# Optimization experiments

Measured on AMD Instinct MI355X. Metric: run time of the kernel, lower is better.

## Reference

```python
import jax, jax.numpy as jnp
import numpy as np

B, N, DIN = 1, 1024, 512
NF, DCOND, H = 4, 128, 8
HD = DIN // H


def layernorm(x, g, b, eps=1e-5):
    mu = jnp.mean(x, axis=-1, keepdims=True)
    var = jnp.var(x, axis=-1, keepdims=True)
    return (x - mu) * jax.lax.rsqrt(var + eps) * g + b


def modlin2d(x, code, w_c, ln_g, ln_b, W, b):
    # code: [dcond, nf]; w_c: [din, dcond] -> code_mod: [nf, 1, din]
    code_mod = layernorm((w_c @ code).T, ln_g, ln_b)[:, None, :]
    return jnp.matmul(x * code_mod, W.T) + b


def setup_inputs() -> dict:
    key = jax.random.key(0)
    ks = jax.random.split(key, 8)
    s = lambda d: 1.0 / np.sqrt(d)
    return {
        "x": jax.random.normal(ks[0], (B, N, DIN), jnp.float32),
        "compatibility": jax.random.uniform(ks[1], (B, NF, N), jnp.float32),
        "code": jax.random.normal(ks[2], (DCOND, NF), jnp.float32),
        "w_c": jax.random.normal(ks[3], (DIN, DCOND), jnp.float32) * s(DCOND),
        "W_qkv": jax.random.normal(ks[4], (3 * DIN, DIN), jnp.float32) * s(DIN),
        "b_qkv": jnp.zeros((3 * DIN,), jnp.float32),
        "W_proj": jax.random.normal(ks[5], (DIN, DIN), jnp.float32) * s(DIN),
        "b_proj": jnp.zeros((DIN,), jnp.float32),
        "ln_qkv_g": jnp.ones((DIN,), jnp.float32),
        "ln_qkv_b": jnp.zeros((DIN,), jnp.float32),
        "ln_proj_g": jnp.ones((DIN,), jnp.float32),
        "ln_proj_b": jnp.zeros((DIN,), jnp.float32),
    }


def reference(x, compatibility, code, w_c, W_qkv, b_qkv, W_proj, b_proj,
              ln_qkv_g, ln_qkv_b, ln_proj_g, ln_proj_b):
    b, n, e = x.shape
    hd = e // H
    scale = hd ** -0.5
    # QKV: [B, nf, N, 3*din] -> split into [3, B, H, nf, N, hd]
    qkv = modlin2d(x[:, None, :, :], code, w_c, ln_qkv_g, ln_qkv_b, W_qkv, b_qkv)
    qkv = qkv.reshape(b, NF, n, 3, H, hd).transpose(3, 0, 4, 1, 2, 5)
    q, k, v = qkv[0], qkv[1], qkv[2]
    # first softmax over scaled scores
    attn = jax.nn.softmax(jnp.einsum('bhfnd,bhfmd->bhfnm', q, k) * scale, axis=-1)
    # compatibility outer product: [B, N, N] (sums over function axis)
    compat = jnp.einsum('bfn,bfm->bnm', compatibility, compatibility)
    W_hat = attn * compat[:, None, None, :, :]
    # second softmax
    Wm = jax.nn.softmax(W_hat, axis=-1)
    y_hat = jnp.einsum('bhfnm,bhfmd->bhfnd', Wm, v)
    y_hat = y_hat.transpose(0, 2, 3, 1, 4).reshape(b, NF, n, e)
    y = modlin2d(y_hat, code, w_c, ln_proj_g, ln_proj_b, W_proj, b_proj)
    return y
```

## Files before the change

### kernel.cpp

```cpp
#include <hip/hip_runtime.h>
#include <hip/hip_bf16.h>
#include <math.h>

#define NTOK 1024
#define DIN  512
#define NF   4
#define DCOND 128
#define H    8
#define HD   64
#define NQKV 1536
#define LOG2E 1.4426950408889634f

typedef __attribute__((ext_vector_type(8))) short bf16x8;
typedef __attribute__((ext_vector_type(4))) float f32x4;
typedef __attribute__((ext_vector_type(4))) unsigned short us4;

__device__ __forceinline__ unsigned short f2b(float f) {
  union { float f; unsigned int u; } v; v.f = f;
  unsigned int r = v.u + 0x7fffu + ((v.u >> 16) & 1u);
  return (unsigned short)(r >> 16);
}

__device__ __forceinline__ float b2f(unsigned short h) {
  union { unsigned int u; float f; } v; v.u = ((unsigned int)h) << 16;
  return v.f;
}

__device__ __forceinline__ float asf(unsigned int u) {
  union { unsigned int u; float f; } v; v.u = u;
  return v.f;
}

__device__ __forceinline__ void gl_lds16(const void* g, void* l) {
  __builtin_amdgcn_global_load_lds(
      (const __attribute__((address_space(1))) unsigned int*)g,
      (__attribute__((address_space(3))) unsigned int*)l, 16, 0, 0);
}

__global__ void ln_kernel(const float* __restrict__ code, const float* __restrict__ w_c,
                          const float* __restrict__ lnqg, const float* __restrict__ lnqb,
                          const float* __restrict__ lnpg, const float* __restrict__ lnpb,
                          float* __restrict__ cmq, float* __restrict__ cmp_) {
  const int i = threadIdx.x;
  const int w = i >> 6, lane = i & 63;
  float t[NF] = {0.f, 0.f, 0.f, 0.f};
  const float* wr = w_c + i * DCOND;
#pragma unroll 8
  for (int k = 0; k < DCOND; k += 4) {
    float4 wv = *reinterpret_cast<const float4*>(wr + k);
    float4 c0 = *reinterpret_cast<const float4*>(&code[k * 4]);
    float4 c1 = *reinterpret_cast<const float4*>(&code[(k + 1) * 4]);
    float4 c2 = *reinterpret_cast<const float4*>(&code[(k + 2) * 4]);
    float4 c3 = *reinterpret_cast<const float4*>(&code[(k + 3) * 4]);
    t[0] += wv.x * c0.x + wv.y * c1.x + wv.z * c2.x + wv.w * c3.x;
    t[1] += wv.x * c0.y + wv.y * c1.y + wv.z * c2.y + wv.w * c3.y;
    t[2] += wv.x * c0.z + wv.y * c1.z + wv.z * c2.z + wv.w * c3.z;
    t[3] += wv.x * c0.w + wv.y * c1.w + wv.z * c2.w + wv.w * c3.w;
  }
  __shared__ float redS[8], redQ[8];
#pragma unroll
  for (int f = 0; f < NF; ++f) {
    float s = t[f], q = t[f] * t[f];
#pragma unroll
    for (int o = 32; o > 0; o >>= 1) { s += __shfl_xor(s, o); q += __shfl_xor(q, o); }
    if (lane == 0) { redS[w] = s; redQ[w] = q; }
    __syncthreads();
    float S = 0.f, Q = 0.f;
#pragma unroll
    for (int j = 0; j < 8; ++j) { S += redS[j]; Q += redQ[j]; }
    float mu = S * (1.f / 512.f);
    float var = Q * (1.f / 512.f) - mu * mu;
    float rstd = rsqrtf(var + 1e-5f);
    float nv = (t[f] - mu) * rstd;
    cmq[f * DIN + i]  = nv * lnqg[i] + lnqb[i];
    cmp_[f * DIN + i] = nv * lnpg[i] + lnpb[i];
    __syncthreads();
  }
}

__global__ void prep2_kernel(const float* __restrict__ W_qkv, const float* __restrict__ W_proj,
                             const float* __restrict__ x, const float* __restrict__ cmq,
                             unsigned short* __restrict__ Wqh, unsigned short* __restrict__ Wph,
                             unsigned short* __restrict__ xm) {
  const int bid = blockIdx.x, tid = threadIdx.x;
  if (bid < 256) {
    const float* src; unsigned short* dst; int e;
    if (bid < 192) { src = W_qkv; dst = Wqh; e = bid * 4096 + tid * 16; }
    else { src = W_proj; dst = Wph; e = (bid - 192) * 4096 + tid * 16; }
#pragma unroll
    for (int j = 0; j < 4; ++j) {
      float4 a = *reinterpret_cast<const float4*>(&src[e + j * 4]);
      us4 p = { f2b(a.x), f2b(a.y), f2b(a.z), f2b(a.w) };
      *reinterpret_cast<us4*>(&dst[e + j * 4]) = p;
    }
  } else {
    int e = (bid - 256) * 4096 + tid * 16;
    int row = e >> 9, d = e & 511;
    int f = row >> 10, n = row & 1023;
    const float* xr = x + (size_t)n * DIN + d;
    const float* cr = cmq + f * DIN + d;
#pragma unroll
    for (int j = 0; j < 4; ++j) {
      float4 a = *reinterpret_cast<const float4*>(xr + j * 4);
      float4 c = *reinterpret_cast<const float4*>(cr + j * 4);
      us4 p = { f2b(a.x * c.x), f2b(a.y * c.y), f2b(a.z * c.z), f2b(a.w * c.w) };
      *reinterpret_cast<us4*>(&xm[e + j * 4]) = p;
    }
  }
}

template<int NCOL, bool OUT_BF16, bool WRITE_VT, bool SCALE_Q>
__global__ __launch_bounds__(256, 6)
void gemm64(const unsigned short* __restrict__ Ah,
            const unsigned short* __restrict__ Wh,
            const float* __restrict__ bias,
            unsigned short* __restrict__ outH,
            float* __restrict__ outF,
            unsigned short* __restrict__ vT) {
  __shared__ __align__(16) unsigned short sA[2][2048];
  __shared__ __align__(16) unsigned short sB[2][2048];
  const int tid = threadIdx.x;
  const int lane = tid & 63, w = tid >> 6;
  const int li = lane & 15, g = lane >> 4;
  const int wr = (w >> 1) * 32, wc = (w & 1) * 32;
  const int row0 = blockIdx.y * 64, col0 = blockIdx.x * 64;
  const int f = row0 >> 10;
  const int sr = tid >> 2, sp = tid & 3;
  const int ss = sp ^ ((sr >> 1) & 3);

  f32x4 acc[2][2];
#pragma unroll
  for (int m = 0; m < 2; ++m)
#pragma unroll
    for (int n = 0; n < 2; ++n) acc[m][n] = (f32x4){0.f, 0.f, 0.f, 0.f};

  const unsigned short* aSrc = Ah + (size_t)(row0 + sr) * DIN + ss * 8;
  const unsigned short* bSrc = Wh + (size_t)(col0 + sr) * DIN + ss * 8;

  gl_lds16(aSrc, &sA[0][w * 512]);
  gl_lds16(bSrc, &sB[0][w * 512]);
  __syncthreads();
  for (int it = 0; it < 16; ++it) {
    int buf = it & 1;
    if (it < 15) {
      gl_lds16(aSrc + (it + 1) * 32, &sA[buf ^ 1][w * 512]);
      gl_lds16(bSrc + (it + 1) * 32, &sB[buf ^ 1][w * 512]);
    }
    bf16x8 aF[2], bF[2];
#pragma unroll
    for (int m = 0; m < 2; ++m) {
      int ra = wr + m * 16 + li;
      aF[m] = *reinterpret_cast<const bf16x8*>(&sA[buf][(ra * 4 + (g ^ ((ra >> 1) & 3))) * 8]);
    }
#pragma unroll
    for (int n = 0; n < 2; ++n) {
      int cb = wc + n * 16 + li;
      bF[n] = *reinterpret_cast<const bf16x8*>(&sB[buf][(cb * 4 + (g ^ ((cb >> 1) & 3))) * 8]);
    }
#pragma unroll
    for (int m = 0; m < 2; ++m)
#pragma unroll
      for (int n = 0; n < 2; ++n)
        acc[m][n] = __builtin_amdgcn_mfma_f32_16x16x32_bf16(aF[m], bF[n], acc[m][n], 0, 0, 0);
    __syncthreads();
  }
#pragma unroll
  for (int n = 0; n < 2; ++n) {
    int col = col0 + wc + n * 16 + li;
    float bb = bias[col];
    float sc = (SCALE_Q && col < DIN) ? (0.125f * LOG2E) : 1.0f;
#pragma unroll
    for (int m = 0; m < 2; ++m) {
      int rb = row0 + wr + m * 16 + g * 4;
      f32x4 v = acc[m][n];
      if constexpr (OUT_BF16) {
        if (WRITE_VT && col >= 1024) {
          int tok0 = rb & 1023;
          us4 pk;
#pragma unroll
          for (int r = 0; r < 4; ++r) pk[r] = f2b(v[r] + bb);
          *reinterpret_cast<us4*>(&vT[((size_t)(f * 512 + (col - 1024))) * NTOK + tok0]) = pk;
        } else {
#pragma unroll
          for (int r = 0; r < 4; ++r)
            outH[(size_t)(rb + r) * NCOL + col] = f2b((v[r] + bb) * sc);
        }
      } else {
#pragma unroll
        for (int r = 0; r < 4; ++r)
          outF[(size_t)(rb + r) * NCOL + col] = v[r] + bb;
      }
    }
  }
}

__global__ __launch_bounds__(512, 4)
void attn_mfma4(const unsigned short* __restrict__ qkvh,
                const unsigned short* __restrict__ vTh,
                const float* __restrict__ comp,
                const float* __restrict__ cmp_,
                unsigned short* __restrict__ ym) {
  __shared__ __align__(16) unsigned short sK[2][4096];
  __shared__ __align__(16) unsigned short sV[2][4096];
  __shared__ __align__(16) unsigned short wbuf_all[8][16 * 68];
  __shared__ unsigned int sc01[1024], sc23[1024];
  __shared__ float lred[2][4][16];
  __shared__ float s2red[4][16];

  const int tid = threadIdx.x, lane = tid & 63, w = tid >> 6;
  const int li = lane & 15, g = lane >> 4;
  const int rt = w & 3, ch = w >> 2;
  const int hf = blockIdx.x, qt = blockIdx.y;
  const int h = hf >> 2, f = hf & 3;

  {
    int c = tid * 2;
    float2 a0 = *reinterpret_cast<const float2*>(&comp[c]);
    float2 a1 = *reinterpret_cast<const float2*>(&comp[1024 + c]);
    float2 a2 = *reinterpret_cast<const float2*>(&comp[2048 + c]);
    float2 a3 = *reinterpret_cast<const float2*>(&comp[3072 + c]);
    sc01[c]     = f2b(a0.x) | ((unsigned int)f2b(a1.x) << 16);
    sc01[c + 1] = f2b(a0.y) | ((unsigned int)f2b(a1.y) << 16);
    sc23[c]     = f2b(a2.x) | ((unsigned int)f2b(a3.x) << 16);
    sc23[c + 1] = f2b(a2.y) | ((unsigned int)f2b(a3.y) << 16);
  }

  const int qrow0 = qt * 64 + rt * 16;
  const unsigned short* qbase = qkvh + ((size_t)(f * NTOK + qrow0 + li)) * NQKV + h * HD;
  bf16x8 aq[2];
  aq[0] = *reinterpret_cast<const bf16x8*>(qbase + g * 8);
  aq[1] = *reinterpret_cast<const bf16x8*>(qbase + 32 + g * 8);

  float crow[4][4];
#pragma unroll
  for (int ff = 0; ff < 4; ++ff)
#pragma unroll
    for (int r = 0; r < 4; ++r)
      crow[ff][r] = comp[ff * NTOK + qrow0 + g * 4 + r];

  const unsigned short* kb = qkvh + ((size_t)(f * NTOK)) * NQKV + DIN + h * HD;
  const unsigned short* vb = vTh + ((size_t)(f * DIN + h * HD)) * NTOK;

  const int remK = w * 64 + lane;
  const int ktok = remK >> 3, kdg = remK & 7;
  const int ksw = kdg ^ (ktok & 7);

  auto stageK_to = [&](unsigned short (*dst)[4096], int s) {
#pragma unroll
    for (int j = 0; j < 2; ++j) {
      int tokg = j * 512 + s * 64 + ktok;
      gl_lds16(kb + (size_t)tokg * NQKV + ksw * 8, &dst[j][(w * 64) * 8]);
    }
  };
  auto stageV_to = [&](int s) {
#pragma unroll
    for (int j = 0; j < 2; ++j) {
      int d = ktok, tg = kdg;
      int sw = tg ^ (d & 7);
      gl_lds16(vb + (size_t)d * NTOK + j * 512 + s * 64 + sw * 8, &sV[j][(w * 64) * 8]);
    }
  };

  float lsum[4] = {0.f, 0.f, 0.f, 0.f};
  stageK_to(sK, 0);
  __syncthreads();
  for (int s = 0; s < 8; ++s) {
    unsigned short (*cur)[4096] = (s & 1) ? sV : sK;
    if (s < 7) stageK_to((s & 1) ? sK : sV, s + 1);
    bf16x8 bk[4][2];
#pragma unroll
    for (int cf = 0; cf < 4; ++cf)
#pragma unroll
      for (int ks = 0; ks < 2; ++ks) {
        int tok = cf * 16 + li, dg = ks * 4 + g;
        bk[cf][ks] = *reinterpret_cast<const bf16x8*>(&cur[ch][(tok * 8 + (dg ^ (tok & 7))) * 8]);
      }
    f32x4 accs[4];
#pragma unroll
    for (int cf = 0; cf < 4; ++cf) accs[cf] = (f32x4){0.f, 0.f, 0.f, 0.f};
#pragma unroll
    for (int ks = 0; ks < 2; ++ks)
#pragma unroll
      for (int cf = 0; cf < 4; ++cf)
        accs[cf] = __builtin_amdgcn_mfma_f32_16x16x32_bf16(aq[ks], bk[cf][ks], accs[cf], 0, 0, 0);
#pragma unroll
    for (int cf = 0; cf < 4; ++cf)
#pragma unroll
      for (int r = 0; r < 4; ++r) lsum[r] += __builtin_amdgcn_exp2f(accs[cf][r]);
    __syncthreads();
  }
#pragma unroll
  for (int r = 0; r < 4; ++r) {
    lsum[r] += __shfl_xor(lsum[r], 1);
    lsum[r] += __shfl_xor(lsum[r], 2);
    lsum[r] += __shfl_xor(lsum[r], 4);
    lsum[r] += __shfl_xor(lsum[r], 8);
  }
  if (li == 0) {
#pragma unroll
    for (int r = 0; r < 4; ++r) lred[ch][rt][g * 4 + r] = lsum[r];
  }
  __syncthreads();
  float invl[4];
#pragma unroll
  for (int r = 0; r < 4; ++r)
    invl[r] = LOG2E / (lred[0][rt][g * 4 + r] + lred[1][rt][g * 4 + r]);

  f32x4 acco[4];
  float sum2[4] = {0.f, 0.f, 0.f, 0.f};
#pragma unroll
  for (int cf = 0; cf < 4; ++cf) acco[cf] = (f32x4){0.f, 0.f, 0.f, 0.f};
  unsigned short* wb = wbuf_all[w];

  stageK_to(sK, 0);
  stageV_to(0);
  __syncthreads();
  for (int s = 0; s < 8; ++s) {
    bf16x8 bk[4][2];
#pragma unroll
    for (int cf = 0; cf < 4; ++cf)
#pragma unroll
      for (int ks = 0; ks < 2; ++ks) {
        int tok = cf * 16 + li, dg = ks * 4 + g;
        bk[cf][ks] = *reinterpret_cast<const bf16x8*>(&sK[ch][(tok * 8 + (dg ^ (tok & 7))) * 8]);
      }
    f32x4 accs[4];
#pragma unroll
    for (int cf = 0; cf < 4; ++cf) accs[cf] = (f32x4){0.f, 0.f, 0.f, 0.f};
#pragma unroll
    for (int ks = 0; ks < 2; ++ks)
#pragma unroll
      for (int cf = 0; cf < 4; ++cf)
        accs[cf] = __builtin_amdgcn_mfma_f32_16x16x32_bf16(aq[ks], bk[cf][ks], accs[cf], 0, 0, 0);
#pragma unroll
    for (int cf = 0; cf < 4; ++cf) {
      int colg = ch * 512 + s * 64 + cf * 16 + li;
      unsigned int u01 = sc01[colg], u23 = sc23[colg];
      float c0 = asf(u01 << 16), c1 = asf(u01 & 0xffff0000u);
      float c2 = asf(u23 << 16), c3 = asf(u23 & 0xffff0000u);
#pragma unroll
      for (int r = 0; r < 4; ++r) {
        float e = __builtin_amdgcn_exp2f(accs[cf][r]);
        float a = e * invl[r];
        float cc = crow[0][r] * c0 + crow[1][r] * c1 + crow[2][r] * c2 + crow[3][r] * c3;
        float tv = __builtin_amdgcn_exp2f(a * cc);
        unsigned short hv = f2b(tv);
        sum2[r] += b2f(hv);
        wb[(g * 4 + r) * 68 + cf * 16 + li] = hv;
      }
    }
    bf16x8 aw[2], bv[4][2];
#pragma unroll
    for (int ks = 0; ks < 2; ++ks)
      aw[ks] = *reinterpret_cast<const bf16x8*>(&wb[li * 68 + ks * 32 + g * 8]);
#pragma unroll
    for (int cf = 0; cf < 4; ++cf)
#pragma unroll
      for (int ks = 0; ks < 2; ++ks) {
        int d = cf * 16 + li, tg = ks * 4 + g;
        bv[cf][ks] = *reinterpret_cast<const bf16x8*>(&sV[ch][(d * 8 + (tg ^ (d & 7))) * 8]);
      }
#pragma unroll
    for (int ks = 0; ks < 2; ++ks)
#pragma unroll
      for (int cf = 0; cf < 4; ++cf)
        acco[cf] = __builtin_amdgcn_mfma_f32_16x16x32_bf16(aw[ks], bv[cf][ks], acco[cf], 0, 0, 0);
    __syncthreads();
    if (s < 7) { stageK_to(sK, s + 1); stageV_to(s + 1); }
    __syncthreads();
  }

#pragma unroll
  for (int r = 0; r < 4; ++r) {
    sum2[r] += __shfl_xor(sum2[r], 1);
    sum2[r] += __shfl_xor(sum2[r], 2);
    sum2[r] += __shfl_xor(sum2[r], 4);
    sum2[r] += __shfl_xor(sum2[r], 8);
  }
  float* fred = (float*)sK;
  __syncthreads();
  if (ch == 1) {
    if (li == 0) {
#pragma unroll
      for (int r = 0; r < 4; ++r) s2red[rt][g * 4 + r] = sum2[r];
    }
#pragma unroll
    for (int cf = 0; cf < 4; ++cf)
#pragma unroll
      for (int r = 0; r < 4; ++r)
        fred[rt * 1024 + (g * 4 + r) * 64 + cf * 16 + li] = acco[cf][r];
  }
  __syncthreads();
  if (ch == 0) {
    float invs[4];
#pragma unroll
    for (int r = 0; r < 4; ++r) invs[r] = 1.f / (sum2[r] + s2red[rt][g * 4 + r]);
    float cscale[4];
#pragma unroll
    for (int cf = 0; cf < 4; ++cf) cscale[cf] = cmp_[f * DIN + h * HD + cf * 16 + li];
#pragma unroll
    for (int cf = 0; cf < 4; ++cf)
#pragma unroll
      for (int r = 0; r < 4; ++r) {
        float v = (acco[cf][r] + fred[rt * 1024 + (g * 4 + r) * 64 + cf * 16 + li]) * invs[r];
        int qrow = qrow0 + g * 4 + r;
        ym[((size_t)(f * NTOK + qrow)) * DIN + h * HD + cf * 16 + li] = f2b(v * cscale[cf]);
      }
  }
}

extern "C" void kernel_launch(void* const* d_in, const int* in_sizes, int n_in,
                              void* d_out, int out_size, void* d_ws, size_t ws_size,
                              hipStream_t stream) {
  const float* x      = (const float*)d_in[0];
  const float* compat = (const float*)d_in[1];
  const float* code   = (const float*)d_in[2];
  const float* w_c    = (const float*)d_in[3];
  const float* W_qkv  = (const float*)d_in[4];
  const float* b_qkv  = (const float*)d_in[5];
  const float* W_proj = (const float*)d_in[6];
  const float* b_proj = (const float*)d_in[7];
  const float* lnqg   = (const float*)d_in[8];
  const float* lnqb   = (const float*)d_in[9];
  const float* lnpg   = (const float*)d_in[10];
  const float* lnpb   = (const float*)d_in[11];
  float* out = (float*)d_out;

  float* cmq  = (float*)d_ws;
  float* cmp_ = cmq + NF * DIN;
  unsigned short* Wqh  = (unsigned short*)(cmp_ + NF * DIN);
  unsigned short* Wph  = Wqh + (size_t)NQKV * DIN;
  unsigned short* xm   = Wph + (size_t)DIN * DIN;
  unsigned short* qkvh = xm + (size_t)NF * NTOK * DIN;
  unsigned short* vTh  = qkvh + (size_t)NF * NTOK * NQKV;
  unsigned short* ym   = vTh + (size_t)NF * DIN * NTOK;

  ln_kernel<<<1, 512, 0, stream>>>(code, w_c, lnqg, lnqb, lnpg, lnpb, cmq, cmp_);
  prep2_kernel<<<768, 256, 0, stream>>>(W_qkv, W_proj, x, cmq, Wqh, Wph, xm);
  gemm64<NQKV, true, true, true><<<dim3(24, 64), 256, 0, stream>>>(
      xm, Wqh, b_qkv, qkvh, nullptr, vTh);
  attn_mfma4<<<dim3(32, 16), 512, 0, stream>>>(qkvh, vTh, compat, cmp_, ym);
  gemm64<DIN, false, false, false><<<dim3(8, 64), 256, 0, stream>>>(
      ym, Wph, b_proj, nullptr, out, nullptr);
}
```

Before: 163.4 us.

## Restructure prep kernels and move attention staging to a single-buffer early-issue scheme

The prep stage is split differently. Weight conversion, the w_c·code matvec (now spread across 8 blocks) and bf16 packing of the compatibility vectors all go into one wide kernel, followed by a tiny layernorm kernel and a separate x-modulation kernel. The attention kernel now reads the pre-packed compatibility from global memory instead of building it in LDS per block. Its K/V staging moves from double buffering (first pass) and end-of-iteration loads (second pass) to a single buffer: the next tile is issued right after the current tile's fragments are read into registers, so the loads overlap the softmax/exp math. This adds an extra kernel launch and extra barriers, and it reads compat from global/L2 inside the inner loop.

```diff
diff --git a/kernel.cpp b/kernel.cpp
--- a/kernel.cpp
+++ b/kernel.cpp
@@ -37,26 +37,50 @@
       (__attribute__((address_space(3))) unsigned int*)l, 16, 0, 0);
 }
 
-__global__ void ln_kernel(const float* __restrict__ code, const float* __restrict__ w_c,
-                          const float* __restrict__ lnqg, const float* __restrict__ lnqb,
-                          const float* __restrict__ lnpg, const float* __restrict__ lnpb,
-                          float* __restrict__ cmq, float* __restrict__ cmp_) {
+__global__ void prep_a(const float* __restrict__ W_qkv, const float* __restrict__ W_proj,
+                       const float* __restrict__ w_c, const float* __restrict__ code,
+                       const float* __restrict__ comp,
+                       unsigned short* __restrict__ Wqh, unsigned short* __restrict__ Wph,
+                       float* __restrict__ tmpv,
+                       unsigned int* __restrict__ cp01, unsigned int* __restrict__ cp23) {
+  const int bid = blockIdx.x, tid = threadIdx.x;
+  if (bid < 256) {
+    const float* src; unsigned short* dst; int e;
+    if (bid < 192) { src = W_qkv; dst = Wqh; e = bid * 4096 + tid * 16; }
+    else { src = W_proj; dst = Wph; e = (bid - 192) * 4096 + tid * 16; }
+#pragma unroll
+    for (int j = 0; j < 4; ++j) {
+      float4 a = *reinterpret_cast<const float4*>(&src[e + j * 4]);
+      us4 p = { f2b(a.x), f2b(a.y), f2b(a.z), f2b(a.w) };
+      *reinterpret_cast<us4*>(&dst[e + j * 4]) = p;
+    }
+  } else if (bid < 264) {
+    int i = (bid - 256) * 64 + (tid >> 2);
+    int f = tid & 3;
+    const float* wr = w_c + i * DCOND;
+    float acc = 0.f;
+#pragma unroll 16
+    for (int k = 0; k < DCOND; ++k) acc += wr[k] * code[k * NF + f];
+    tmpv[f * DIN + i] = acc;
+  } else {
+#pragma unroll
+    for (int j = 0; j < 4; ++j) {
+      int c = tid * 4 + j;
+      cp01[c] = (unsigned int)f2b(comp[c]) | ((unsigned int)f2b(comp[1024 + c]) << 16);
+      cp23[c] = (unsigned int)f2b(comp[2048 + c]) | ((unsigned int)f2b(comp[3072 + c]) << 16);
+    }
+  }
+}
+
+__global__ void ln2_kernel(const float* __restrict__ tmpv,
+                           const float* __restrict__ lnqg, const float* __restrict__ lnqb,
+                           const float* __restrict__ lnpg, const float* __restrict__ lnpb,
+                           float* __restrict__ cmq, float* __restrict__ cmp_) {
   const int i = threadIdx.x;
   const int w = i >> 6, lane = i & 63;
-  float t[NF] = {0.f, 0.f, 0.f, 0.f};
-  const float* wr = w_c + i * DCOND;
-#pragma unroll 8
-  for (int k = 0; k < DCOND; k += 4) {
-    float4 wv = *reinterpret_cast<const float4*>(wr + k);
-    float4 c0 = *reinterpret_cast<const float4*>(&code[k * 4]);
-    float4 c1 = *reinterpret_cast<const float4*>(&code[(k + 1) * 4]);
-    float4 c2 = *reinterpret_cast<const float4*>(&code[(k + 2) * 4]);
-    float4 c3 = *reinterpret_cast<const float4*>(&code[(k + 3) * 4]);
-    t[0] += wv.x * c0.x + wv.y * c1.x + wv.z * c2.x + wv.w * c3.x;
-    t[1] += wv.x * c0.y + wv.y * c1.y + wv.z * c2.y + wv.w * c3.y;
-    t[2] += wv.x * c0.z + wv.y * c1.z + wv.z * c2.z + wv.w * c3.z;
-    t[3] += wv.x * c0.w + wv.y * c1.w + wv.z * c2.w + wv.w * c3.w;
-  }
+  float t[NF];
+#pragma unroll
+  for (int f = 0; f < NF; ++f) t[f] = tmpv[f * DIN + i];
   __shared__ float redS[8], redQ[8];
 #pragma unroll
   for (int f = 0; f < NF; ++f) {
@@ -78,34 +102,19 @@
   }
 }
 
-__global__ void prep2_kernel(const float* __restrict__ W_qkv, const float* __restrict__ W_proj,
-                             const float* __restrict__ x, const float* __restrict__ cmq,
-                             unsigned short* __restrict__ Wqh, unsigned short* __restrict__ Wph,
-                             unsigned short* __restrict__ xm) {
-  const int bid = blockIdx.x, tid = threadIdx.x;
-  if (bid < 256) {
-    const float* src; unsigned short* dst; int e;
-    if (bid < 192) { src = W_qkv; dst = Wqh; e = bid * 4096 + tid * 16; }
-    else { src = W_proj; dst = Wph; e = (bid - 192) * 4096 + tid * 16; }
-#pragma unroll
-    for (int j = 0; j < 4; ++j) {
-      float4 a = *reinterpret_cast<const float4*>(&src[e + j * 4]);
-      us4 p = { f2b(a.x), f2b(a.y), f2b(a.z), f2b(a.w) };
-      *reinterpret_cast<us4*>(&dst[e + j * 4]) = p;
-    }
-  } else {
-    int e = (bid - 256) * 4096 + tid * 16;
-    int row = e >> 9, d = e & 511;
-    int f = row >> 10, n = row & 1023;
-    const float* xr = x + (size_t)n * DIN + d;
-    const float* cr = cmq + f * DIN + d;
-#pragma unroll
-    for (int j = 0; j < 4; ++j) {
-      float4 a = *reinterpret_cast<const float4*>(xr + j * 4);
-      float4 c = *reinterpret_cast<const float4*>(cr + j * 4);
-      us4 p = { f2b(a.x * c.x), f2b(a.y * c.y), f2b(a.z * c.z), f2b(a.w * c.w) };
-      *reinterpret_cast<us4*>(&xm[e + j * 4]) = p;
-    }
+__global__ void prep_b(const float* __restrict__ x, const float* __restrict__ cmq,
+                       unsigned short* __restrict__ xm) {
+  int e = blockIdx.x * 4096 + threadIdx.x * 16;
+  int row = e >> 9, d = e & 511;
+  int f = row >> 10, n = row & 1023;
+  const float* xr = x + (size_t)n * DIN + d;
+  const float* cr = cmq + f * DIN + d;
+#pragma unroll
+  for (int j = 0; j < 4; ++j) {
+    float4 a = *reinterpret_cast<const float4*>(xr + j * 4);
+    float4 c = *reinterpret_cast<const float4*>(cr + j * 4);
+    us4 p = { f2b(a.x * c.x), f2b(a.y * c.y), f2b(a.z * c.z), f2b(a.w * c.w) };
+    *reinterpret_cast<us4*>(&xm[e + j * 4]) = p;
   }
 }
 
@@ -195,15 +204,16 @@
 }
 
 __global__ __launch_bounds__(512, 4)
-void attn_mfma4(const unsigned short* __restrict__ qkvh,
+void attn_mfma5(const unsigned short* __restrict__ qkvh,
                 const unsigned short* __restrict__ vTh,
                 const float* __restrict__ comp,
+                const unsigned int* __restrict__ cp01,
+                const unsigned int* __restrict__ cp23,
                 const float* __restrict__ cmp_,
                 unsigned short* __restrict__ ym) {
   __shared__ __align__(16) unsigned short sK[2][4096];
   __shared__ __align__(16) unsigned short sV[2][4096];
   __shared__ __align__(16) unsigned short wbuf_all[8][16 * 68];
-  __shared__ unsigned int sc01[1024], sc23[1024];
   __shared__ float lred[2][4][16];
   __shared__ float s2red[4][16];
 
@@ -213,18 +223,6 @@
   const int hf = blockIdx.x, qt = blockIdx.y;
   const int h = hf >> 2, f = hf & 3;
 
-  {
-    int c = tid * 2;
-    float2 a0 = *reinterpret_cast<const float2*>(&comp[c]);
-    float2 a1 = *reinterpret_cast<const float2*>(&comp[1024 + c]);
-    float2 a2 = *reinterpret_cast<const float2*>(&comp[2048 + c]);
-    float2 a3 = *reinterpret_cast<const float2*>(&comp[3072 + c]);
-    sc01[c]     = f2b(a0.x) | ((unsigned int)f2b(a1.x) << 16);
-    sc01[c + 1] = f2b(a0.y) | ((unsigned int)f2b(a1.y) << 16);
-    sc23[c]     = f2b(a2.x) | ((unsigned int)f2b(a3.x) << 16);
-    sc23[c + 1] = f2b(a2.y) | ((unsigned int)f2b(a3.y) << 16);
-  }
-
   const int qrow0 = qt * 64 + rt * 16;
   const unsigned short* qbase = qkvh + ((size_t)(f * NTOK + qrow0 + li)) * NQKV + h * HD;
   bf16x8 aq[2];
@@ -245,14 +243,14 @@
   const int ktok = remK >> 3, kdg = remK & 7;
   const int ksw = kdg ^ (ktok & 7);
 
-  auto stageK_to = [&](unsigned short (*dst)[4096], int s) {
+  auto stageK = [&](int s) {
 #pragma unroll
     for (int j = 0; j < 2; ++j) {
       int tokg = j * 512 + s * 64 + ktok;
-      gl_lds16(kb + (size_t)tokg * NQKV + ksw * 8, &dst[j][(w * 64) * 8]);
+      gl_lds16(kb + (size_t)tokg * NQKV + ksw * 8, &sK[j][(w * 64) * 8]);
     }
   };
-  auto stageV_to = [&](int s) {
+  auto stageV = [&](int s) {
 #pragma unroll
     for (int j = 0; j < 2; ++j) {
       int d = ktok, tg = kdg;
@@ -262,18 +260,16 @@
   };
 
   float lsum[4] = {0.f, 0.f, 0.f, 0.f};
-  stageK_to(sK, 0);
+  stageK(0);
   __syncthreads();
   for (int s = 0; s < 8; ++s) {
-    unsigned short (*cur)[4096] = (s & 1) ? sV : sK;
-    if (s < 7) stageK_to((s & 1) ? sK : sV, s + 1);
     bf16x8 bk[4][2];
 #pragma unroll
     for (int cf = 0; cf < 4; ++cf)
 #pragma unroll
       for (int ks = 0; ks < 2; ++ks) {
         int tok = cf * 16 + li, dg = ks * 4 + g;
-        bk[cf][ks] = *reinterpret_cast<const bf16x8*>(&cur[ch][(tok * 8 + (dg ^ (tok & 7))) * 8]);
+        bk[cf][ks] = *reinterpret_cast<const bf16x8*>(&sK[ch][(tok * 8 + (dg ^ (tok & 7))) * 8]);
       }
     f32x4 accs[4];
 #pragma unroll
@@ -283,6 +279,8 @@
 #pragma unroll
       for (int cf = 0; cf < 4; ++cf)
         accs[cf] = __builtin_amdgcn_mfma_f32_16x16x32_bf16(aq[ks], bk[cf][ks], accs[cf], 0, 0, 0);
+    __syncthreads();
+    if (s < 7) stageK(s + 1);
 #pragma unroll
     for (int cf = 0; cf < 4; ++cf)
 #pragma unroll
@@ -312,8 +310,8 @@
   for (int cf = 0; cf < 4; ++cf) acco[cf] = (f32x4){0.f, 0.f, 0.f, 0.f};
   unsigned short* wb = wbuf_all[w];
 
-  stageK_to(sK, 0);
-  stageV_to(0);
+  stageK(0);
+  stageV(0);
   __syncthreads();
   for (int s = 0; s < 8; ++s) {
     bf16x8 bk[4][2];
@@ -332,10 +330,20 @@
 #pragma unroll
       for (int cf = 0; cf < 4; ++cf)
         accs[cf] = __builtin_amdgcn_mfma_f32_16x16x32_bf16(aq[ks], bk[cf][ks], accs[cf], 0, 0, 0);
+    bf16x8 bv[4][2];
+#pragma unroll
+    for (int cf = 0; cf < 4; ++cf)
+#pragma unroll
+      for (int ks = 0; ks < 2; ++ks) {
+        int d = cf * 16 + li, tg = ks * 4 + g;
+        bv[cf][ks] = *reinterpret_cast<const bf16x8*>(&sV[ch][(d * 8 + (tg ^ (d & 7))) * 8]);
+      }
+    __syncthreads();
+    if (s < 7) { stageK(s + 1); stageV(s + 1); }
 #pragma unroll
     for (int cf = 0; cf < 4; ++cf) {
       int colg = ch * 512 + s * 64 + cf * 16 + li;
-      unsigned int u01 = sc01[colg], u23 = sc23[colg];
+      unsigned int u01 = cp01[colg], u23 = cp23[colg];
       float c0 = asf(u01 << 16), c1 = asf(u01 & 0xffff0000u);
       float c2 = asf(u23 << 16), c3 = asf(u23 & 0xffff0000u);
 #pragma unroll
@@ -349,24 +357,15 @@
         wb[(g * 4 + r) * 68 + cf * 16 + li] = hv;
       }
     }
-    bf16x8 aw[2], bv[4][2];
+    bf16x8 aw[2];
 #pragma unroll
     for (int ks = 0; ks < 2; ++ks)
       aw[ks] = *reinterpret_cast<const bf16x8*>(&wb[li * 68 + ks * 32 + g * 8]);
 #pragma unroll
-    for (int cf = 0; cf < 4; ++cf)
-#pragma unroll
-      for (int ks = 0; ks < 2; ++ks) {
-        int d = cf * 16 + li, tg = ks * 4 + g;
-        bv[cf][ks] = *reinterpret_cast<const bf16x8*>(&sV[ch][(d * 8 + (tg ^ (d & 7))) * 8]);
-      }
-#pragma unroll
     for (int ks = 0; ks < 2; ++ks)
 #pragma unroll
       for (int cf = 0; cf < 4; ++cf)
         acco[cf] = __builtin_amdgcn_mfma_f32_16x16x32_bf16(aw[ks], bv[cf][ks], acco[cf], 0, 0, 0);
-    __syncthreads();
-    if (s < 7) { stageK_to(sK, s + 1); stageV_to(s + 1); }
     __syncthreads();
   }
 
@@ -434,12 +433,17 @@
   unsigned short* qkvh = xm + (size_t)NF * NTOK * DIN;
   unsigned short* vTh  = qkvh + (size_t)NF * NTOK * NQKV;
   unsigned short* ym   = vTh + (size_t)NF * DIN * NTOK;
-
-  ln_kernel<<<1, 512, 0, stream>>>(code, w_c, lnqg, lnqb, lnpg, lnpb, cmq, cmp_);
-  prep2_kernel<<<768, 256, 0, stream>>>(W_qkv, W_proj, x, cmq, Wqh, Wph, xm);
+  float* tmpv = (float*)(ym + (size_t)NF * NTOK * DIN);
+  unsigned int* cp01 = (unsigned int*)(tmpv + NF * DIN);
+  unsigned int* cp23 = cp01 + NTOK;
+
+  prep_a<<<265, 256, 0, stream>>>(W_qkv, W_proj, w_c, code, compat,
+                                  Wqh, Wph, tmpv, cp01, cp23);
+  ln2_kernel<<<1, 512, 0, stream>>>(tmpv, lnqg, lnqb, lnpg, lnpb, cmq, cmp_);
+  prep_b<<<512, 256, 0, stream>>>(x, cmq, xm);
   gemm64<NQKV, true, true, true><<<dim3(24, 64), 256, 0, stream>>>(
       xm, Wqh, b_qkv, qkvh, nullptr, vTh);
-  attn_mfma4<<<dim3(32, 16), 512, 0, stream>>>(qkvh, vTh, compat, cmp_, ym);
+  attn_mfma5<<<dim3(32, 16), 512, 0, stream>>>(qkvh, vTh, compat, cp01, cp23, cmp_, ym);
   gemm64<DIN, false, false, false><<<dim3(8, 64), 256, 0, stream>>>(
       ym, Wph, b_proj, nullptr, out, nullptr);
 }
```

Result: slower. 171.2 us (+4.8%).

## Parallelize code projection across blocks and overlap next K/V staging with softmax

Applied to the files above, without the earlier changes.

The w_c@code projection moves out of the single-block LN kernel and becomes a parallel part of the weight-conversion kernel. A small LN kernel then normalizes the result, and a separate kernel builds the modulated x. In the attention loop, V fragments are now loaded into registers right after the QK MFMAs, so the next tile's K/V staging can start before the exp/compat/softmax math instead of after the PV MFMAs. This aims to hide load latency and shorten the serial single-block prep, at the cost of one extra kernel launch and more registers held live.

```diff
diff --git a/kernel.cpp b/kernel.cpp
--- a/kernel.cpp
+++ b/kernel.cpp
@@ -37,26 +37,41 @@
       (__attribute__((address_space(3))) unsigned int*)l, 16, 0, 0);
 }
 
-__global__ void ln_kernel(const float* __restrict__ code, const float* __restrict__ w_c,
-                          const float* __restrict__ lnqg, const float* __restrict__ lnqb,
-                          const float* __restrict__ lnpg, const float* __restrict__ lnpb,
-                          float* __restrict__ cmq, float* __restrict__ cmp_) {
+__global__ void prep_a(const float* __restrict__ W_qkv, const float* __restrict__ W_proj,
+                       const float* __restrict__ w_c, const float* __restrict__ code,
+                       unsigned short* __restrict__ Wqh, unsigned short* __restrict__ Wph,
+                       float* __restrict__ tmpv) {
+  const int bid = blockIdx.x, tid = threadIdx.x;
+  if (bid < 256) {
+    const float* src; unsigned short* dst; int e;
+    if (bid < 192) { src = W_qkv; dst = Wqh; e = bid * 4096 + tid * 16; }
+    else { src = W_proj; dst = Wph; e = (bid - 192) * 4096 + tid * 16; }
+#pragma unroll
+    for (int j = 0; j < 4; ++j) {
+      float4 a = *reinterpret_cast<const float4*>(&src[e + j * 4]);
+      us4 p = { f2b(a.x), f2b(a.y), f2b(a.z), f2b(a.w) };
+      *reinterpret_cast<us4*>(&dst[e + j * 4]) = p;
+    }
+  } else {
+    int i = (bid - 256) * 64 + (tid >> 2);
+    int f = tid & 3;
+    const float* wr = w_c + i * DCOND;
+    float acc = 0.f;
+#pragma unroll 16
+    for (int k = 0; k < DCOND; ++k) acc += wr[k] * code[k * NF + f];
+    tmpv[f * DIN + i] = acc;
+  }
+}
+
+__global__ void ln2_kernel(const float* __restrict__ tmpv,
+                           const float* __restrict__ lnqg, const float* __restrict__ lnqb,
+                           const float* __restrict__ lnpg, const float* __restrict__ lnpb,
+                           float* __restrict__ cmq, float* __restrict__ cmp_) {
   const int i = threadIdx.x;
   const int w = i >> 6, lane = i & 63;
-  float t[NF] = {0.f, 0.f, 0.f, 0.f};
-  const float* wr = w_c + i * DCOND;
-#pragma unroll 8
-  for (int k = 0; k < DCOND; k += 4) {
-    float4 wv = *reinterpret_cast<const float4*>(wr + k);
-    float4 c0 = *reinterpret_cast<const float4*>(&code[k * 4]);
-    float4 c1 = *reinterpret_cast<const float4*>(&code[(k + 1) * 4]);
-    float4 c2 = *reinterpret_cast<const float4*>(&code[(k + 2) * 4]);
-    float4 c3 = *reinterpret_cast<const float4*>(&code[(k + 3) * 4]);
-    t[0] += wv.x * c0.x + wv.y * c1.x + wv.z * c2.x + wv.w * c3.x;
-    t[1] += wv.x * c0.y + wv.y * c1.y + wv.z * c2.y + wv.w * c3.y;
-    t[2] += wv.x * c0.z + wv.y * c1.z + wv.z * c2.z + wv.w * c3.z;
-    t[3] += wv.x * c0.w + wv.y * c1.w + wv.z * c2.w + wv.w * c3.w;
-  }
+  float t[NF];
+#pragma unroll
+  for (int f = 0; f < NF; ++f) t[f] = tmpv[f * DIN + i];
   __shared__ float redS[8], redQ[8];
 #pragma unroll
   for (int f = 0; f < NF; ++f) {
@@ -78,34 +93,19 @@
   }
 }
 
-__global__ void prep2_kernel(const float* __restrict__ W_qkv, const float* __restrict__ W_proj,
-                             const float* __restrict__ x, const float* __restrict__ cmq,
-                             unsigned short* __restrict__ Wqh, unsigned short* __restrict__ Wph,
-                             unsigned short* __restrict__ xm) {
-  const int bid = blockIdx.x, tid = threadIdx.x;
-  if (bid < 256) {
-    const float* src; unsigned short* dst; int e;
-    if (bid < 192) { src = W_qkv; dst = Wqh; e = bid * 4096 + tid * 16; }
-    else { src = W_proj; dst = Wph; e = (bid - 192) * 4096 + tid * 16; }
-#pragma unroll
-    for (int j = 0; j < 4; ++j) {
-      float4 a = *reinterpret_cast<const float4*>(&src[e + j * 4]);
-      us4 p = { f2b(a.x), f2b(a.y), f2b(a.z), f2b(a.w) };
-      *reinterpret_cast<us4*>(&dst[e + j * 4]) = p;
-    }
-  } else {
-    int e = (bid - 256) * 4096 + tid * 16;
-    int row = e >> 9, d = e & 511;
-    int f = row >> 10, n = row & 1023;
-    const float* xr = x + (size_t)n * DIN + d;
-    const float* cr = cmq + f * DIN + d;
-#pragma unroll
-    for (int j = 0; j < 4; ++j) {
-      float4 a = *reinterpret_cast<const float4*>(xr + j * 4);
-      float4 c = *reinterpret_cast<const float4*>(cr + j * 4);
-      us4 p = { f2b(a.x * c.x), f2b(a.y * c.y), f2b(a.z * c.z), f2b(a.w * c.w) };
-      *reinterpret_cast<us4*>(&xm[e + j * 4]) = p;
-    }
+__global__ void prep_b(const float* __restrict__ x, const float* __restrict__ cmq,
+                       unsigned short* __restrict__ xm) {
+  int e = blockIdx.x * 4096 + threadIdx.x * 16;
+  int row = e >> 9, d = e & 511;
+  int f = row >> 10, n = row & 1023;
+  const float* xr = x + (size_t)n * DIN + d;
+  const float* cr = cmq + f * DIN + d;
+#pragma unroll
+  for (int j = 0; j < 4; ++j) {
+    float4 a = *reinterpret_cast<const float4*>(xr + j * 4);
+    float4 c = *reinterpret_cast<const float4*>(cr + j * 4);
+    us4 p = { f2b(a.x * c.x), f2b(a.y * c.y), f2b(a.z * c.z), f2b(a.w * c.w) };
+    *reinterpret_cast<us4*>(&xm[e + j * 4]) = p;
   }
 }
 
@@ -195,7 +195,7 @@
 }
 
 __global__ __launch_bounds__(512, 4)
-void attn_mfma4(const unsigned short* __restrict__ qkvh,
+void attn_mfma6(const unsigned short* __restrict__ qkvh,
                 const unsigned short* __restrict__ vTh,
                 const float* __restrict__ comp,
                 const float* __restrict__ cmp_,
@@ -332,6 +332,16 @@
 #pragma unroll
       for (int cf = 0; cf < 4; ++cf)
         accs[cf] = __builtin_amdgcn_mfma_f32_16x16x32_bf16(aq[ks], bk[cf][ks], accs[cf], 0, 0, 0);
+    bf16x8 bv[4][2];
+#pragma unroll
+    for (int cf = 0; cf < 4; ++cf)
+#pragma unroll
+      for (int ks = 0; ks < 2; ++ks) {
+        int d = cf * 16 + li, tg = ks * 4 + g;
+        bv[cf][ks] = *reinterpret_cast<const bf16x8*>(&sV[ch][(d * 8 + (tg ^ (d & 7))) * 8]);
+      }
+    __syncthreads();
+    if (s < 7) { stageK_to(sK, s + 1); stageV_to(s + 1); }
 #pragma unroll
     for (int cf = 0; cf < 4; ++cf) {
       int colg = ch * 512 + s * 64 + cf * 16 + li;
@@ -349,24 +359,15 @@
         wb[(g * 4 + r) * 68 + cf * 16 + li] = hv;
       }
     }
-    bf16x8 aw[2], bv[4][2];
+    bf16x8 aw[2];
 #pragma unroll
     for (int ks = 0; ks < 2; ++ks)
       aw[ks] = *reinterpret_cast<const bf16x8*>(&wb[li * 68 + ks * 32 + g * 8]);
 #pragma unroll
-    for (int cf = 0; cf < 4; ++cf)
-#pragma unroll
-      for (int ks = 0; ks < 2; ++ks) {
-        int d = cf * 16 + li, tg = ks * 4 + g;
-        bv[cf][ks] = *reinterpret_cast<const bf16x8*>(&sV[ch][(d * 8 + (tg ^ (d & 7))) * 8]);
-      }
-#pragma unroll
     for (int ks = 0; ks < 2; ++ks)
 #pragma unroll
       for (int cf = 0; cf < 4; ++cf)
         acco[cf] = __builtin_amdgcn_mfma_f32_16x16x32_bf16(aw[ks], bv[cf][ks], acco[cf], 0, 0, 0);
-    __syncthreads();
-    if (s < 7) { stageK_to(sK, s + 1); stageV_to(s + 1); }
     __syncthreads();
   }
 
@@ -434,12 +435,14 @@
   unsigned short* qkvh = xm + (size_t)NF * NTOK * DIN;
   unsigned short* vTh  = qkvh + (size_t)NF * NTOK * NQKV;
   unsigned short* ym   = vTh + (size_t)NF * DIN * NTOK;
-
-  ln_kernel<<<1, 512, 0, stream>>>(code, w_c, lnqg, lnqb, lnpg, lnpb, cmq, cmp_);
-  prep2_kernel<<<768, 256, 0, stream>>>(W_qkv, W_proj, x, cmq, Wqh, Wph, xm);
+  float* tmpv = (float*)(ym + (size_t)NF * NTOK * DIN);
+
+  prep_a<<<264, 256, 0, stream>>>(W_qkv, W_proj, w_c, code, Wqh, Wph, tmpv);
+  ln2_kernel<<<1, 512, 0, stream>>>(tmpv, lnqg, lnqb, lnpg, lnpb, cmq, cmp_);
+  prep_b<<<512, 256, 0, stream>>>(x, cmq, xm);
   gemm64<NQKV, true, true, true><<<dim3(24, 64), 256, 0, stream>>>(
       xm, Wqh, b_qkv, qkvh, nullptr, vTh);
-  attn_mfma4<<<dim3(32, 16), 512, 0, stream>>>(qkvh, vTh, compat, cmp_, ym);
+  attn_mfma6<<<dim3(32, 16), 512, 0, stream>>>(qkvh, vTh, compat, cmp_, ym);
   gemm64<DIN, false, false, false><<<dim3(8, 64), 256, 0, stream>>>(
       ym, Wph, b_proj, nullptr, out, nullptr);
 }
```

Result: slower. 172.7 us (+5.7%).
